# Optimization experiments

Hardware: AMD Instinct MI355X
Metric: run time of the kernel (lower is better)

## Reference

```python
import jax, jax.numpy as jnp
import numpy as np

STRIDE = (2, 2)
PADDING = (1, 1)
DILATION = (1, 1)
KERNEL = (3, 3)


def _out_hw(h_in, w_in):
    h_out = (h_in + 2 * PADDING[0] - DILATION[0] * (KERNEL[0] - 1) - 1) // STRIDE[0] + 1
    w_out = (w_in + 2 * PADDING[1] - DILATION[1] * (KERNEL[1] - 1) - 1) // STRIDE[1] + 1
    return h_out, w_out


def _stride_permutation(h_out, w_out):
    # Single-shot multiplexing row permutation (mirrors _get_stride_permutation).
    s_h, s_w = STRIDE
    if s_h == 1 and s_w == 1:
        return np.arange(h_out * w_out)
    perm = []
    for si in range(s_h):
        for sj in range(s_w):
            for i in range((h_out + s_h - 1) // s_h):
                ai = i * s_h + si
                if ai >= h_out:
                    continue
                for j in range((w_out + s_w - 1) // s_w):
                    aj = j * s_w + sj
                    if aj >= w_out:
                        continue
                    perm.append(ai * w_out + aj)
    return np.asarray(perm, dtype=np.int32)


def setup_inputs() -> dict:
    key = jax.random.key(0)
    kx, kw, kb = jax.random.split(key, 3)
    x = jax.random.normal(kx, (16, 256, 64, 64), dtype=jnp.float32)
    weight = jax.random.normal(kw, (256, 256, 3, 3), dtype=jnp.float32)
    bias = jax.random.normal(kb, (256,), dtype=jnp.float32)
    return {"x": x, "weight": weight, "bias": bias}


def reference(x, weight, bias):
    # Toeplitz matrix-vector product == grouped strided conv.
    out = jax.lax.conv_general_dilated(
        x, weight,
        window_strides=STRIDE,
        padding=[(PADDING[0], PADDING[0]), (PADDING[1], PADDING[1])],
        rhs_dilation=DILATION,
        dimension_numbers=("NCHW", "OIHW", "NCHW"),
        feature_group_count=1,
    )  # [B, Cout, h_out, w_out]
    b, c, h_out, w_out = out.shape
    perm = jnp.asarray(_stride_permutation(h_out, w_out))
    flat = out.reshape(b, c, h_out * w_out)
    # permuted[new_idx] = flat[perm[new_idx]] (single-shot stride multiplexing)
    permuted = flat[:, :, perm]
    return permuted + bias[None, :, None]
```

## Files before the change

kernel.cpp:

```cpp
#include <hip/hip_runtime.h>
#include <cstdint>

typedef __attribute__((ext_vector_type(8))) __bf16 bf16x8;
typedef __attribute__((ext_vector_type(4))) float f32x4;
typedef __attribute__((ext_vector_type(4))) uint32_t u32x4;

#define NB   16
#define CIN  256
#define COUT 256
#define HP   66
#define WP   66
#define KTOT 2304
#define XPB  (HP*WP*256)
#define XPAD_ELEMS (NB*XPB)

__device__ __forceinline__ uint16_t f2bf(float f) {
  uint32_t u = __builtin_bit_cast(uint32_t, f);
  u = (u + 0x7FFFu + ((u >> 16) & 1u)) >> 16;
  return (uint16_t)u;
}

__global__ void prep_kernel(const float* __restrict__ x, const float* __restrict__ w,
                            uint16_t* __restrict__ xpad, uint16_t* __restrict__ bw) {
  const int bid = blockIdx.x;
  const int tid = threadIdx.x;
  if (bid < 2048) {
    const int lane = tid & 63;
    const int wvi = tid >> 6;
    const int chalf = bid & 1;
    const int h = (bid >> 1) & 63;
    const int b = bid >> 7;
    const int cg = lane >> 4;
    const int w4 = (lane & 15) * 4;
    const int c0 = chalf * 128 + wvi * 32 + cg * 8;
    const float* src = x + ((size_t)(b * 256 + c0) * 64 + h) * 64 + w4;
    f32x4 v[8];
    #pragma unroll
    for (int j = 0; j < 8; ++j)
      v[j] = *(const f32x4*)(src + (size_t)j * 4096);
    uint16_t* dst = xpad + ((size_t)(b * HP + h + 1) * WP + 1 + w4) * 256 + c0;
    #pragma unroll
    for (int p = 0; p < 4; ++p) {
      u32x4 d;
      #pragma unroll
      for (int k = 0; k < 4; ++k)
        d[k] = (uint32_t)f2bf(v[2 * k][p]) | ((uint32_t)f2bf(v[2 * k + 1][p]) << 16);
      *(u32x4*)(dst + p * 256) = d;
    }
  } else if (bid < 3088) {
    const int idx = (bid - 2048) * 256 + tid;
    const int b = idx / 16640;
    const int r = idx - b * 16640;
    uint64_t* base = (uint64_t*)(xpad + (size_t)b * XPB);
    int off;
    if (r < 4224) {
      off = r;
    } else if (r < 8448) {
      off = 274560 + (r - 4224);
    } else if (r < 12544) {
      const int i = r - 8448;
      off = (1 + (i >> 6)) * 4224 + (i & 63);
    } else {
      const int i = r - 12544;
      off = (1 + (i >> 6)) * 4224 + 4160 + (i & 63);
    }
    base[off] = 0;
  } else {
    const int gid = (bid - 3088) * 256 + tid;
    const int co = gid / 288;
    const int r = gid - co * 288;
    const int tap = r >> 5;
    const int ci0 = (r & 31) * 8;
    u32x4 d;
    #pragma unroll
    for (int k = 0; k < 4; ++k) {
      const float v0 = w[((co * 256 + ci0 + 2 * k + 0) * 9) + tap];
      const float v1 = w[((co * 256 + ci0 + 2 * k + 1) * 9) + tap];
      d[k] = (uint32_t)f2bf(v0) | ((uint32_t)f2bf(v1) << 16);
    }
    *(u32x4*)(bw + co * KTOT + tap * 256 + ci0) = d;
  }
}

__device__ __forceinline__ void gl_lds16(const void* g, void* l) {
  __builtin_amdgcn_global_load_lds(
      (__attribute__((address_space(1))) void*)(uintptr_t)g,
      (__attribute__((address_space(3))) void*)(uint32_t)(uintptr_t)l,
      16, 0, 0);
}

__global__ __launch_bounds__(256, 2) void gemm_kernel(
    const uint16_t* __restrict__ xpad, const uint16_t* __restrict__ bw,
    const float* __restrict__ bias, float* __restrict__ out) {
  __shared__ uint16_t lA[2][128 * 64];
  const int tid = threadIdx.x;
  const int wv = tid >> 6, lane = tid & 63;
  const int quad = lane >> 4, l15 = lane & 15, l7 = lane & 7;
  const int wm = wv >> 1, wn = wv & 1;

  const int xcd = blockIdx.x & 7;
  const int grp = blockIdx.x >> 3;
  const int mtile = xcd * 16 + (grp >> 2);
  const int ntile = grp & 3;
  const int n0 = ntile * 64;
  const int m0 = mtile * 128;
  const int bidx = m0 >> 10;
  const int q0 = m0 & 1023;

  int a_goff[4];
  #pragma unroll
  for (int t = 0; t < 4; ++t) {
    const int slot = t * 256 + tid;
    const int row = slot >> 3;
    const int kc = (slot & 7) ^ (row & 7);
    const int p = q0 + row;
    const int oh = 2 * ((p >> 4) & 15) + ((p >> 9) & 1);
    const int ow = 2 * (p & 15) + ((p >> 8) & 1);
    a_goff[t] = ((bidx * HP + 2 * oh) * WP + 2 * ow) * 256 + kc * 8;
  }

  const uint16_t* bcol0 = bw + (size_t)(n0 + wn * 32 + 0 * 16 + l15) * KTOT + quad * 8;
  const uint16_t* bcol1 = bw + (size_t)(n0 + wn * 32 + 1 * 16 + l15) * KTOT + quad * 8;

  #define AOFF(r, s) ((wm * 64 + (r) * 16 + l15) * 128 + ((((s) * 4 + quad) ^ l7) * 16))
  const int aoff00 = AOFF(0, 0), aoff01 = AOFF(0, 1);
  const int aoff10 = AOFF(1, 0), aoff11 = AOFF(1, 1);
  const int aoff20 = AOFF(2, 0), aoff21 = AOFF(2, 1);
  const int aoff30 = AOFF(3, 0), aoff31 = AOFF(3, 1);
  #undef AOFF

  f32x4 acc00{0,0,0,0}, acc01{0,0,0,0};
  f32x4 acc10{0,0,0,0}, acc11{0,0,0,0};
  f32x4 acc20{0,0,0,0}, acc21{0,0,0,0};
  f32x4 acc30{0,0,0,0}, acc31{0,0,0,0};

  auto stageA = [&](int it, int buf) {
    const int tap = it >> 2;
    const int kh = tap / 3, kw = tap - kh * 3;
    const int ci0 = (it & 3) << 6;
    const uint16_t* aptr = xpad + (kh * WP + kw) * 256 + ci0;
    char* la_ = (char*)&lA[buf][0];
    #pragma unroll
    for (int t = 0; t < 4; ++t)
      gl_lds16(aptr + a_goff[t], la_ + (t * 256 + wv * 64) * 16);
  };

  #define LOADB(it, R0, R1, R2, R3) do {                                        \
    const int _ko = ((it) >> 2) * 256 + (((it) & 3) << 6);                      \
    R0 = *(const bf16x8*)(bcol0 + _ko);  R1 = *(const bf16x8*)(bcol0 + _ko + 32); \
    R2 = *(const bf16x8*)(bcol1 + _ko);  R3 = *(const bf16x8*)(bcol1 + _ko + 32); \
  } while (0)

  #define MFMA __builtin_amdgcn_mfma_f32_16x16x32_bf16
  #define COMPUTE(buf, R0, R1, R2, R3) do {                                     \
    const char* _la = (const char*)&lA[buf][0];                                 \
    bf16x8 _a0 = *(const bf16x8*)(_la + aoff00);                                \
    bf16x8 _a1 = *(const bf16x8*)(_la + aoff10);                                \
    bf16x8 _a2 = *(const bf16x8*)(_la + aoff20);                                \
    bf16x8 _a3 = *(const bf16x8*)(_la + aoff30);                                \
    acc00 = MFMA(_a0, R0, acc00, 0,0,0);  acc01 = MFMA(_a0, R2, acc01, 0,0,0);  \
    acc10 = MFMA(_a1, R0, acc10, 0,0,0);  acc11 = MFMA(_a1, R2, acc11, 0,0,0);  \
    acc20 = MFMA(_a2, R0, acc20, 0,0,0);  acc21 = MFMA(_a2, R2, acc21, 0,0,0);  \
    acc30 = MFMA(_a3, R0, acc30, 0,0,0);  acc31 = MFMA(_a3, R2, acc31, 0,0,0);  \
    _a0 = *(const bf16x8*)(_la + aoff01);                                       \
    _a1 = *(const bf16x8*)(_la + aoff11);                                       \
    _a2 = *(const bf16x8*)(_la + aoff21);                                       \
    _a3 = *(const bf16x8*)(_la + aoff31);                                       \
    acc00 = MFMA(_a0, R1, acc00, 0,0,0);  acc01 = MFMA(_a0, R3, acc01, 0,0,0);  \
    acc10 = MFMA(_a1, R1, acc10, 0,0,0);  acc11 = MFMA(_a1, R3, acc11, 0,0,0);  \
    acc20 = MFMA(_a2, R1, acc20, 0,0,0);  acc21 = MFMA(_a2, R3, acc21, 0,0,0);  \
    acc30 = MFMA(_a3, R1, acc30, 0,0,0);  acc31 = MFMA(_a3, R3, acc31, 0,0,0);  \
  } while (0)

  bf16x8 pa0, pa1, pa2, pa3;
  bf16x8 pb0, pb1, pb2, pb3;

  stageA(0, 0);
  LOADB(0, pa0, pa1, pa2, pa3);

  for (int ih = 0; ih < 17; ++ih) {
    __syncthreads();
    stageA(2 * ih + 1, 1);
    LOADB(2 * ih + 1, pb0, pb1, pb2, pb3);
    COMPUTE(0, pa0, pa1, pa2, pa3);
    __syncthreads();
    stageA(2 * ih + 2, 0);
    LOADB(2 * ih + 2, pa0, pa1, pa2, pa3);
    COMPUTE(1, pb0, pb1, pb2, pb3);
  }
  __syncthreads();
  stageA(35, 1);
  LOADB(35, pb0, pb1, pb2, pb3);
  COMPUTE(0, pa0, pa1, pa2, pa3);
  __syncthreads();
  COMPUTE(1, pb0, pb1, pb2, pb3);

  float* obase = out + (size_t)bidx * (COUT * 1024);
  #define STORE(r, c, A) do {                                                   \
    const int _co = n0 + wn * 32 + (c) * 16 + l15;                              \
    const int _q  = q0 + wm * 64 + (r) * 16 + quad * 4;                         \
    f32x4 _v = A; _v += bias[_co];                                              \
    *(f32x4*)(obase + (size_t)_co * 1024 + _q) = _v;                            \
  } while (0)
  STORE(0, 0, acc00); STORE(0, 1, acc01);
  STORE(1, 0, acc10); STORE(1, 1, acc11);
  STORE(2, 0, acc20); STORE(2, 1, acc21);
  STORE(3, 0, acc30); STORE(3, 1, acc31);
  #undef STORE
  #undef COMPUTE
  #undef LOADB
  #undef MFMA
}

extern "C" void kernel_launch(void* const* d_in, const int* in_sizes, int n_in,
                              void* d_out, int out_size, void* d_ws, size_t ws_size,
                              hipStream_t stream) {
  const float* x    = (const float*)d_in[0];
  const float* w    = (const float*)d_in[1];
  const float* bias = (const float*)d_in[2];
  float* out = (float*)d_out;
  uint16_t* xpad = (uint16_t*)d_ws;
  uint16_t* bwq  = xpad + XPAD_ELEMS;

  prep_kernel<<<dim3(3376), dim3(256), 0, stream>>>(x, w, xpad, bwq);
  gemm_kernel<<<dim3(512), dim3(256), 0, stream>>>(xpad, bwq, bias, out);
}
```

Before: 150.8 us.

## Triple-buffer LDS A tiles with partial vmcnt waits instead of syncthreads

```diff
diff --git a/kernel.cpp b/kernel.cpp
--- a/kernel.cpp
+++ b/kernel.cpp
@@ -92,7 +92,7 @@
 __global__ __launch_bounds__(256, 2) void gemm_kernel(
     const uint16_t* __restrict__ xpad, const uint16_t* __restrict__ bw,
     const float* __restrict__ bias, float* __restrict__ out) {
-  __shared__ uint16_t lA[2][128 * 64];
+  __shared__ uint16_t lA[3][128 * 64];
   const int tid = threadIdx.x;
   const int wv = tid >> 6, lane = tid & 63;
   const int quad = lane >> 4, l15 = lane & 15, l7 = lane & 7;
@@ -176,24 +176,49 @@
   bf16x8 pb0, pb1, pb2, pb3;
 
   stageA(0, 0);
+  stageA(1, 1);
   LOADB(0, pa0, pa1, pa2, pa3);
 
+  int buf = 0;
   for (int ih = 0; ih < 17; ++ih) {
-    __syncthreads();
-    stageA(2 * ih + 1, 1);
-    LOADB(2 * ih + 1, pb0, pb1, pb2, pb3);
-    COMPUTE(0, pa0, pa1, pa2, pa3);
-    __syncthreads();
-    stageA(2 * ih + 2, 0);
-    LOADB(2 * ih + 2, pa0, pa1, pa2, pa3);
-    COMPUTE(1, pb0, pb1, pb2, pb3);
+    {
+      const int it = 2 * ih;
+      asm volatile("s_waitcnt vmcnt(8)" ::: "memory");
+      __builtin_amdgcn_s_barrier();
+      asm volatile("" ::: "memory");
+      int bnext = buf + 2; if (bnext >= 3) bnext -= 3;
+      stageA(it + 2, bnext);
+      LOADB(it + 1, pb0, pb1, pb2, pb3);
+      COMPUTE(buf, pa0, pa1, pa2, pa3);
+      buf = (buf == 2) ? 0 : buf + 1;
+    }
+    {
+      const int it = 2 * ih + 1;
+      asm volatile("s_waitcnt vmcnt(8)" ::: "memory");
+      __builtin_amdgcn_s_barrier();
+      asm volatile("" ::: "memory");
+      if (it < 33) {
+        int bnext = buf + 2; if (bnext >= 3) bnext -= 3;
+        stageA(it + 2, bnext);
+      } else {
+        int bnext = buf + 2; if (bnext >= 3) bnext -= 3;
+        stageA(35, bnext);
+      }
+      LOADB(it + 1, pa0, pa1, pa2, pa3);
+      COMPUTE(buf, pb0, pb1, pb2, pb3);
+      buf = (buf == 2) ? 0 : buf + 1;
+    }
   }
-  __syncthreads();
-  stageA(35, 1);
+  asm volatile("s_waitcnt vmcnt(8)" ::: "memory");
+  __builtin_amdgcn_s_barrier();
+  asm volatile("" ::: "memory");
   LOADB(35, pb0, pb1, pb2, pb3);
-  COMPUTE(0, pa0, pa1, pa2, pa3);
-  __syncthreads();
-  COMPUTE(1, pb0, pb1, pb2, pb3);
+  COMPUTE(buf, pa0, pa1, pa2, pa3);
+  buf = (buf == 2) ? 0 : buf + 1;
+  asm volatile("s_waitcnt vmcnt(8)" ::: "memory");
+  __builtin_amdgcn_s_barrier();
+  asm volatile("" ::: "memory");
+  COMPUTE(buf, pb0, pb1, pb2, pb3);
 
   float* obase = out + (size_t)bidx * (COUT * 1024);
   #define STORE(r, c, A) do {                                                   \
```

Result: slower. 153.8 us (+2.0%).
